# Optimization experiments

Measured on AMD Instinct MI355X. Metric: run time of the kernel, lower is better.

## Reference

```python
import jax, jax.numpy as jnp
import numpy as np

DIM = 192
WIN = 7
HEADS = 6
SHIFT = 3
HID = 4 * DIM


def _ln(x, w, b, eps=1e-5):
    m = jnp.mean(x, axis=-1, keepdims=True)
    v = jnp.var(x, axis=-1, keepdims=True)
    return (x - m) * jax.lax.rsqrt(v + eps) * w + b


def setup_inputs() -> dict:
    key = jax.random.key(0)
    ks = jax.random.split(key, 8)
    B, C, H, W = 16, DIM, 56, 56
    s = lambda k, shape, fan: jax.random.normal(k, shape, jnp.float32) * (1.0 / np.sqrt(fan))
    return {
        "x": jax.random.normal(ks[0], (B, C, H, W), jnp.float32),
        "norm1_w": jnp.ones((C,), jnp.float32),
        "norm1_b": jnp.zeros((C,), jnp.float32),
        "qkv_w": s(ks[1], (3 * C, C), C),
        "qkv_b": jnp.zeros((3 * C,), jnp.float32),
        "proj_w": s(ks[2], (C, C), C),
        "proj_b": jnp.zeros((C,), jnp.float32),
        "norm2_w": jnp.ones((C,), jnp.float32),
        "norm2_b": jnp.zeros((C,), jnp.float32),
        "fc1_w": s(ks[3], (HID, C), C),
        "fc1_b": jnp.zeros((HID,), jnp.float32),
        "fc2_w": s(ks[4], (C, HID), HID),
        "fc2_b": jnp.zeros((C,), jnp.float32),
    }


def reference(x, norm1_w, norm1_b, qkv_w, qkv_b, proj_w, proj_b,
              norm2_w, norm2_b, fc1_w, fc1_b, fc2_w, fc2_b):
    B, C, H, W = x.shape
    shift = SHIFT if (H > WIN and W > WIN) else 0
    shortcut = x

    xl = jnp.transpose(x, (0, 2, 3, 1))            # B,H,W,C
    xl = _ln(xl, norm1_w, norm1_b)
    if shift > 0:
        xl = jnp.roll(xl, shift=(-shift, -shift), axis=(1, 2))
    nH, nW = H // WIN, W // WIN
    xw = xl.reshape(B, nH, WIN, nW, WIN, C)
    xw = jnp.transpose(xw, (0, 1, 3, 2, 4, 5)).reshape(-1, WIN * WIN, C)

    # window attention
    Bw, N, _ = xw.shape
    dh = C // HEADS
    qkv = jnp.einsum('bnc,oc->bno', xw, qkv_w) + qkv_b
    qkv = qkv.reshape(Bw, N, 3, HEADS, dh)
    q, k, v = qkv[:, :, 0], qkv[:, :, 1], qkv[:, :, 2]   # Bw,N,H,dh
    scale = dh ** -0.5
    attn = jnp.einsum('bnhd,bmhd->bhnm', q, k) * scale
    attn = jax.nn.softmax(attn, axis=-1)
    out = jnp.einsum('bhnm,bmhd->bnhd', attn, v).reshape(Bw, N, C)
    out = jnp.einsum('bnc,oc->bno', out, proj_w) + proj_b

    # window reverse -> B,H,W,C
    xl = out.reshape(B, nH, nW, WIN, WIN, C)
    xl = jnp.transpose(xl, (0, 1, 3, 2, 4, 5)).reshape(B, H, W, C)
    if shift > 0:
        xl = jnp.roll(xl, shift=(shift, shift), axis=(1, 2))

    # norm2 + MLP (note: original has NO attention residual)
    xl = _ln(xl, norm2_w, norm2_b)
    h = jnp.einsum('bhwc,oc->bhwo', xl, fc1_w) + fc1_b
    h = jax.nn.gelu(h, approximate=False)
    h = jnp.einsum('bhwo,co->bhwc', h, fc2_w) + fc2_b
    return jnp.transpose(h, (0, 3, 1, 2)) + shortcut
```

## Files before the change

### kernel.cpp

```cpp
#include <hip/hip_runtime.h>
#include <hip/hip_bf16.h>

typedef __bf16 bf16_t;
typedef __bf16 bf16x4 __attribute__((ext_vector_type(4)));
typedef __bf16 bf16x8 __attribute__((ext_vector_type(8)));
typedef float f32x4 __attribute__((ext_vector_type(4)));

#define MFMA16(a, b, c) __builtin_amdgcn_mfma_f32_16x16x32_bf16((a), (b), (c), 0, 0, 0)

__device__ __forceinline__ void gl16(const bf16_t* g, void* l) {
    __builtin_amdgcn_global_load_lds(
        (const __attribute__((address_space(1))) void*)g,
        (__attribute__((address_space(3))) void*)l, 16, 0, 0);
}


__global__ __launch_bounds__(256) void k_cvt(const float* __restrict__ qkvw,
                                             const float* __restrict__ projw,
                                             const float* __restrict__ fc1w,
                                             const float* __restrict__ fc2w,
                                             bf16_t* __restrict__ dst)
{
    int i = blockIdx.x * 256 + threadIdx.x;
    if (i >= 442368) return;
    float v;
    if (i < 110592)      v = qkvw[i];
    else if (i < 147456) v = projw[i - 110592];
    else if (i < 294912) v = fc1w[i - 147456];
    else                 v = fc2w[i - 294912];
    dst[i] = (bf16_t)v;
}

__global__ __launch_bounds__(1024) void k_ln1(const float* __restrict__ x,
                                              const float* __restrict__ gam,
                                              const float* __restrict__ bet,
                                              bf16_t* __restrict__ xw)
{
    __shared__ float tile[56][193];
    __shared__ bf16_t obuf[56 * 192];
    const int bh = blockIdx.x;
    const int b = bh / 56, h = bh % 56;
    const int tid = threadIdx.x;

    {
        const int g = tid >> 4, u = tid & 15;
        const float* xb = x + (long)b * 602112 + (long)h * 56;
        if (u < 14) {
            #pragma unroll
            for (int k = 0; k < 3; ++k) {
                const int c = g + 64 * k;
                float4 v = *(const float4*)(xb + (long)c * 3136 + u * 4);
                tile[u * 4 + 0][c] = v.x;
                tile[u * 4 + 1][c] = v.y;
                tile[u * 4 + 2][c] = v.z;
                tile[u * 4 + 3][c] = v.w;
            }
        }
    }
    __syncthreads();

    const int wave = tid >> 6, lane = tid & 63;
    const float g0 = gam[lane], g1 = gam[lane + 64], g2 = gam[lane + 128];
    const float b0 = bet[lane], b1 = bet[lane + 64], b2 = bet[lane + 128];
    for (int wp = wave; wp < 56; wp += 16) {
        float v0 = tile[wp][lane], v1 = tile[wp][lane + 64], v2 = tile[wp][lane + 128];
        float s = v0 + v1 + v2;
        float sq = v0 * v0 + v1 * v1 + v2 * v2;
        #pragma unroll
        for (int d = 1; d < 64; d <<= 1) { s += __shfl_xor(s, d); sq += __shfl_xor(sq, d); }
        float mean = s * (1.f / 192.f);
        float var  = sq * (1.f / 192.f) - mean * mean;
        float rs = rsqrtf(var + 1e-5f);
        const int wr = (wp + 53) % 56;
        bf16_t* o = obuf + wr * 192;
        o[lane]       = (bf16_t)((v0 - mean) * rs * g0 + b0);
        o[lane + 64]  = (bf16_t)((v1 - mean) * rs * g1 + b1);
        o[lane + 128] = (bf16_t)((v2 - mean) * rs * g2 + b2);
    }
    __syncthreads();

    const int hr = (h + 53) % 56;
    const int nh = hr / 7, ii = hr % 7;
    const long rband = ((long)b * 64 + (long)nh * 8) * 49 + (long)ii * 7;
    const int4* src = (const int4*)obuf;
    for (int q = tid; q < 1344; q += 1024) {
        const int g = q / 168, u = q % 168;
        const int jj = u / 24, ci = u % 24;
        const long r = rband + (long)g * 49 + jj;
        ((int4*)xw)[r * 24 + ci] = src[(g * 7 + jj) * 24 + ci];
    }
}

template<int EPI>
__global__ __launch_bounds__(256) void k_gemm(const bf16_t* __restrict__ A,
                                              const bf16_t* __restrict__ W,
                                              const float* __restrict__ bias,
                                              bf16_t* __restrict__ outp,
                                              int M, int N, int K)
{
    __shared__ bf16_t As[128][64];
    __shared__ bf16_t Bs[64][64];
    const int tid = threadIdx.x;
    const int wv = tid >> 6, ln = tid & 63;
    const int lrow = ln & 15, lkg = ln >> 4;
    const int r7 = lrow & 7;
    const int wm = (wv >> 1) * 64, wn = (wv & 1) * 32;
    const long m0 = (long)blockIdx.x * 128;
    const int n0 = blockIdx.y * 64;

    f32x4 acc[4][2];
    #pragma unroll
    for (int mi = 0; mi < 4; ++mi)
        #pragma unroll
        for (int ni = 0; ni < 2; ++ni)
            #pragma unroll
            for (int rg = 0; rg < 4; ++rg) acc[mi][ni][rg] = 0.f;

    for (int k0 = 0; k0 < K; k0 += 64) {
        #pragma unroll
        for (int i = 0; i < 4; ++i) {
            const int off = ((wv * 4 + i) << 10) + ln * 16;
            const int row = off >> 7, c16 = (off >> 4) & 7;
            gl16(A + (m0 + row) * K + k0 + ((c16 ^ (row & 7)) << 3),
                 (char*)As + ((wv * 4 + i) << 10));
        }
        #pragma unroll
        for (int i = 0; i < 2; ++i) {
            const int off = ((wv * 2 + i) << 10) + ln * 16;
            const int row = off >> 7, c16 = (off >> 4) & 7;
            gl16(W + (long)(n0 + row) * K + k0 + ((c16 ^ (row & 7)) << 3),
                 (char*)Bs + ((wv * 2 + i) << 10));
        }
        __syncthreads();
        #pragma unroll
        for (int kk = 0; kk < 2; ++kk) {
            bf16x8 af[4], bfr[2];
            #pragma unroll
            for (int mi = 0; mi < 4; ++mi) {
                const int row = wm + mi * 16 + lrow;
                af[mi] = *(const bf16x8*)((const char*)As + row * 128
                           + ((((kk << 2) | lkg) ^ r7) << 4));
            }
            #pragma unroll
            for (int ni = 0; ni < 2; ++ni) {
                const int row = wn + ni * 16 + lrow;
                bfr[ni] = *(const bf16x8*)((const char*)Bs + row * 128
                           + ((((kk << 2) | lkg) ^ r7) << 4));
            }
            #pragma unroll
            for (int mi = 0; mi < 4; ++mi)
                #pragma unroll
                for (int ni = 0; ni < 2; ++ni)
                    acc[mi][ni] = MFMA16(bfr[ni], af[mi], acc[mi][ni]);
        }
        __syncthreads();
    }

    #pragma unroll
    for (int mi = 0; mi < 4; ++mi) {
        const long m = m0 + wm + mi * 16 + lrow;
        #pragma unroll
        for (int ni = 0; ni < 2; ++ni) {
            const int nb = n0 + wn + ni * 16 + lkg * 4;
            const float4 bv = *(const float4*)(bias + nb);
            float v[4] = { acc[mi][ni][0] + bv.x, acc[mi][ni][1] + bv.y,
                           acc[mi][ni][2] + bv.z, acc[mi][ni][3] + bv.w };
            bf16x4 o;
            #pragma unroll
            for (int rg = 0; rg < 4; ++rg) {
                float t = v[rg];
                if (EPI == 2) {
                    float t2 = fminf(t * (1.5957691216057308f
                                          + 0.07135481627f * t * t), 60.f);
                    float e = __expf(t2);
                    t = t * e / (e + 1.f);
                }
                o[rg] = (bf16_t)t;
            }
            *(bf16x4*)(outp + m * N + nb) = o;
        }
    }
}

__global__ __launch_bounds__(256) void k_proj_ln(const bf16_t* __restrict__ A,
                                                 const bf16_t* __restrict__ W,
                                                 const float* __restrict__ bias,
                                                 const float* __restrict__ gam,
                                                 const float* __restrict__ bet,
                                                 bf16_t* __restrict__ out)
{
    __shared__ bf16_t As[128][72];
    __shared__ bf16_t Bs[192][72];
    const int tid = threadIdx.x;
    const int wave = tid >> 6, lane = tid & 63;
    const int lrow = lane & 15, lkg = lane >> 4;
    const int wm = wave * 32;
    const long m0 = (long)blockIdx.x * 128;

    f32x4 acc[2][12];
    #pragma unroll
    for (int mi = 0; mi < 2; ++mi)
        #pragma unroll
        for (int ni = 0; ni < 12; ++ni)
            #pragma unroll
            for (int rg = 0; rg < 4; ++rg) acc[mi][ni][rg] = 0.f;

    for (int k0 = 0; k0 < 192; k0 += 64) {
        #pragma unroll
        for (int it = 0; it < 4; ++it) {
            int e = (tid + it * 256) * 8;
            int r = e >> 6, c = e & 63;
            *(int4*)(&As[r][c]) = *(const int4*)(A + (m0 + r) * 192 + (k0 + c));
        }
        #pragma unroll
        for (int it = 0; it < 6; ++it) {
            int e = (tid + it * 256) * 8;
            int r = e >> 6, c = e & 63;
            *(int4*)(&Bs[r][c]) = *(const int4*)(W + (long)r * 192 + (k0 + c));
        }
        __syncthreads();
        #pragma unroll
        for (int kk = 0; kk < 64; kk += 32) {
            bf16x8 af[2];
            #pragma unroll
            for (int mi = 0; mi < 2; ++mi)
                af[mi] = *(const bf16x8*)(&As[wm + mi * 16 + lrow][kk + lkg * 8]);
            #pragma unroll
            for (int ni = 0; ni < 12; ++ni) {
                bf16x8 bfr = *(const bf16x8*)(&Bs[ni * 16 + lrow][kk + lkg * 8]);
                acc[0][ni] = MFMA16(af[0], bfr, acc[0][ni]);
                acc[1][ni] = MFMA16(af[1], bfr, acc[1][ni]);
            }
        }
        __syncthreads();
    }

    float bv[12];
    #pragma unroll
    for (int ni = 0; ni < 12; ++ni) bv[ni] = bias[ni * 16 + lrow];

    #pragma unroll
    for (int mi = 0; mi < 2; ++mi) {
        #pragma unroll
        for (int rg = 0; rg < 4; ++rg) {
            float val[12];
            float s = 0.f, sq = 0.f;
            #pragma unroll
            for (int ni = 0; ni < 12; ++ni) {
                val[ni] = acc[mi][ni][rg] + bv[ni];
                s += val[ni];
                sq += val[ni] * val[ni];
            }
            #pragma unroll
            for (int d = 1; d < 16; d <<= 1) {
                s += __shfl_xor(s, d);
                sq += __shfl_xor(sq, d);
            }
            float mean = s * (1.f / 192.f);
            float var  = sq * (1.f / 192.f) - mean * mean;
            float rs = rsqrtf(var + 1e-5f);
            const long row = m0 + wm + mi * 16 + lkg * 4 + rg;
            bf16_t* orow = out + row * 192;
            #pragma unroll
            for (int ni = 0; ni < 12; ++ni) {
                const int col = ni * 16 + lrow;
                orow[col] = (bf16_t)((val[ni] - mean) * rs * gam[col] + bet[col]);
            }
        }
    }
}

__global__ __launch_bounds__(64) void k_attn(const bf16_t* __restrict__ qkv,
                                             bf16_t* __restrict__ aout)
{
    __shared__ bf16_t Pl[64][72];
    __shared__ bf16_t Vt[32][72];
    const int win = blockIdx.x, head = blockIdx.y;
    const int lane = threadIdx.x;
    const int lrow = lane & 15, lkg = lane >> 4;
    const bf16_t* base = qkv + (long)win * 28224 + head * 32;

    {
        const int m = lane;
        const int mc = (m < 49) ? m : 48;
        const int4* vr = (const int4*)(base + (long)mc * 576 + 384);
        #pragma unroll
        for (int c4 = 0; c4 < 4; ++c4) {
            int4 vv = vr[c4];
            if (m >= 49) vv = make_int4(0, 0, 0, 0);
            const bf16_t* pe = (const bf16_t*)&vv;
            #pragma unroll
            for (int e = 0; e < 8; ++e) Vt[c4 * 8 + e][m] = pe[e];
        }
    }

    bf16x8 z8;
    #pragma unroll
    for (int e = 0; e < 8; ++e) z8[e] = (bf16_t)0.f;
    bf16x8 qf[4], kf[4];
    #pragma unroll
    for (int t = 0; t < 4; ++t) {
        const int n = t * 16 + lrow;
        const int nc = (n < 49) ? n : 48;
        bf16x8 qv = *(const bf16x8*)(base + (long)nc * 576 + lkg * 8);
        bf16x8 kv = *(const bf16x8*)(base + (long)nc * 576 + 192 + lkg * 8);
        qf[t] = (n < 49) ? qv : z8;
        kf[t] = (n < 49) ? kv : z8;
    }
    f32x4 zf; zf[0] = zf[1] = zf[2] = zf[3] = 0.f;
    f32x4 S[4][4];
    #pragma unroll
    for (int mi = 0; mi < 4; ++mi)
        #pragma unroll
        for (int mj = 0; mj < 4; ++mj)
            S[mi][mj] = MFMA16(qf[mi], kf[mj], zf);

    const float scl = 0.17677669529663687f;
    #pragma unroll
    for (int mi = 0; mi < 4; ++mi) {
        #pragma unroll
        for (int rg = 0; rg < 4; ++rg) {
            float v0 = S[mi][0][rg] * scl;
            float v1 = S[mi][1][rg] * scl;
            float v2 = S[mi][2][rg] * scl;
            float v3 = (lrow == 0) ? S[mi][3][rg] * scl : -1e30f;
            float mx = fmaxf(fmaxf(v0, v1), fmaxf(v2, v3));
            #pragma unroll
            for (int d = 1; d < 16; d <<= 1) mx = fmaxf(mx, __shfl_xor(mx, d));
            float e0 = expf(v0 - mx), e1 = expf(v1 - mx), e2 = expf(v2 - mx);
            float e3 = (lrow == 0) ? expf(v3 - mx) : 0.f;
            float sm = e0 + e1 + e2 + e3;
            #pragma unroll
            for (int d = 1; d < 16; d <<= 1) sm += __shfl_xor(sm, d);
            float is = 1.f / sm;
            const int row = mi * 16 + lkg * 4 + rg;
            Pl[row][lrow]      = (bf16_t)(e0 * is);
            Pl[row][16 + lrow] = (bf16_t)(e1 * is);
            Pl[row][32 + lrow] = (bf16_t)(e2 * is);
            Pl[row][48 + lrow] = (bf16_t)(e3 * is);
        }
    }
    __syncthreads();

    f32x4 o[4][2];
    #pragma unroll
    for (int ni = 0; ni < 4; ++ni)
        #pragma unroll
        for (int di = 0; di < 2; ++di)
            #pragma unroll
            for (int rg = 0; rg < 4; ++rg) o[ni][di][rg] = 0.f;
    #pragma unroll
    for (int m0 = 0; m0 < 64; m0 += 32) {
        bf16x8 pf[4], vf[2];
        #pragma unroll
        for (int ni = 0; ni < 4; ++ni)
            pf[ni] = *(const bf16x8*)(&Pl[ni * 16 + lrow][m0 + lkg * 8]);
        #pragma unroll
        for (int di = 0; di < 2; ++di)
            vf[di] = *(const bf16x8*)(&Vt[di * 16 + lrow][m0 + lkg * 8]);
        #pragma unroll
        for (int ni = 0; ni < 4; ++ni)
            #pragma unroll
            for (int di = 0; di < 2; ++di)
                o[ni][di] = MFMA16(pf[ni], vf[di], o[ni][di]);
    }
    #pragma unroll
    for (int ni = 0; ni < 4; ++ni) {
        #pragma unroll
        for (int rg = 0; rg < 4; ++rg) {
            const int n = ni * 16 + lkg * 4 + rg;
            if (n < 49) {
                bf16_t* orow = aout + ((long)win * 49 + n) * 192 + head * 32;
                orow[lrow]      = (bf16_t)o[ni][0][rg];
                orow[16 + lrow] = (bf16_t)o[ni][1][rg];
            }
        }
    }
}

__global__ __launch_bounds__(1024) void k_final(const bf16_t* __restrict__ fb,
                                                const float* __restrict__ x,
                                                float* __restrict__ out)
{
    __shared__ float tile[56][199];
    const int bh = blockIdx.x;
    const int b = bh / 56, hq = bh % 56;
    const int tid = threadIdx.x;
    const int hr = (hq + 53) % 56;
    const int nh = hr / 7, ii = hr % 7;
    const long rband = ((long)b * 64 + (long)nh * 8) * 49 + (long)ii * 7;

    for (int q = tid; q < 1344; q += 1024) {
        const int g = q / 168, rem = q % 168;
        const int jj = rem / 24, ci = rem % 24;
        const long rr = rband + (long)g * 49 + jj;
        bf16x8 v = *(const bf16x8*)(fb + rr * 192 + ci * 8);
        const int wq = (g * 7 + jj + 3) % 56;
        #pragma unroll
        for (int e = 0; e < 8; ++e) tile[wq][ci * 8 + e] = (float)v[e];
    }
    __syncthreads();

    const int g = tid >> 4, u = tid & 15;
    if (u < 14) {
        #pragma unroll
        for (int k = 0; k < 3; ++k) {
            const int c = g + 64 * k;
            const long base = ((long)b * 192 + c) * 3136 + (long)hq * 56 + u * 4;
            float4 xv = *(const float4*)(x + base);
            float4 ov;
            ov.x = tile[u * 4 + 0][c] + xv.x;
            ov.y = tile[u * 4 + 1][c] + xv.y;
            ov.z = tile[u * 4 + 2][c] + xv.z;
            ov.w = tile[u * 4 + 3][c] + xv.w;
            *(float4*)(out + base) = ov;
        }
    }
}

extern "C" void kernel_launch(void* const* d_in, const int* in_sizes, int n_in,
                              void* d_out, int out_size, void* d_ws, size_t ws_size,
                              hipStream_t stream)
{
    const float* x     = (const float*)d_in[0];
    const float* n1w   = (const float*)d_in[1];
    const float* n1b   = (const float*)d_in[2];
    const float* qkvw  = (const float*)d_in[3];
    const float* qkvb  = (const float*)d_in[4];
    const float* projw = (const float*)d_in[5];
    const float* projb = (const float*)d_in[6];
    const float* n2w   = (const float*)d_in[7];
    const float* n2b   = (const float*)d_in[8];
    const float* fc1w  = (const float*)d_in[9];
    const float* fc1b  = (const float*)d_in[10];
    const float* fc2w  = (const float*)d_in[11];
    const float* fc2b  = (const float*)d_in[12];

    char* ws = (char*)d_ws;
    bf16_t* wqkv  = (bf16_t*)(ws);
    bf16_t* wproj = (bf16_t*)(ws + 221184);
    bf16_t* wfc1  = (bf16_t*)(ws + 294912);
    bf16_t* wfc2  = (bf16_t*)(ws + 589824);
    bf16_t* Xb    = (bf16_t*)(ws + 884736);
    bf16_t* QKV   = (bf16_t*)(ws + 20152320);
    bf16_t* Hb    = (bf16_t*)(ws + 77955072);
    bf16_t* H2    = (bf16_t*)(ws + 155025408);
    bf16_t* X2    = (bf16_t*)(ws + 174292992);

    k_cvt<<<1728, 256, 0, stream>>>(qkvw, projw, fc1w, fc2w, wqkv);
    k_ln1<<<896, 1024, 0, stream>>>(x, n1w, n1b, Xb);
    k_gemm<0><<<dim3(392, 9), 256, 0, stream>>>(Xb, wqkv, qkvb, QKV, 50176, 576, 192);
    k_attn<<<dim3(1024, 6), 64, 0, stream>>>(QKV, Xb);
    k_proj_ln<<<392, 256, 0, stream>>>(Xb, wproj, projb, n2w, n2b, X2);
    k_gemm<2><<<dim3(392, 12), 256, 0, stream>>>(X2, wfc1, fc1b, Hb, 50176, 768, 192);
    k_gemm<0><<<dim3(392, 3), 256, 0, stream>>>(Hb, wfc2, fc2b, H2, 50176, 192, 768);
    k_final<<<896, 1024, 0, stream>>>(H2, x, (float*)d_out);
}
```

Before: 219.7 us.

## Double-buffer GEMM LDS tiles and process several M tiles per block

Makes the GEMM kernel double-buffered: the next K tile (or the next M tile's first K tile) is loaded into a second LDS buffer while the current one is computed, leaving one barrier per step. For the K=192 GEMMs each block now handles four consecutive 128-row M tiles and writes the epilogue between them, so the grid shrinks fourfold. N and K become template constants. This hides global-load latency behind MFMA work and lowers per-block launch overhead, but doubles LDS use (possibly lowering occupancy) and gives fewer blocks for the QKV and fc1 launches.

```diff
diff --git a/kernel.cpp b/kernel.cpp
--- a/kernel.cpp
+++ b/kernel.cpp
@@ -91,23 +91,39 @@
     }
 }
 
-template<int EPI>
+template<int EPI, int N, int K, int G>
 __global__ __launch_bounds__(256) void k_gemm(const bf16_t* __restrict__ A,
                                               const bf16_t* __restrict__ W,
                                               const float* __restrict__ bias,
-                                              bf16_t* __restrict__ outp,
-                                              int M, int N, int K)
-{
-    __shared__ bf16_t As[128][64];
-    __shared__ bf16_t Bs[64][64];
+                                              bf16_t* __restrict__ outp)
+{
+    constexpr int NT = K / 64;
+    constexpr int NS = G * NT;
+    __shared__ bf16_t As[2][128 * 64];
+    __shared__ bf16_t Bs[2][64 * 64];
     const int tid = threadIdx.x;
     const int wv = tid >> 6, ln = tid & 63;
     const int lrow = ln & 15, lkg = ln >> 4;
     const int r7 = lrow & 7;
     const int wm = (wv >> 1) * 64, wn = (wv & 1) * 32;
-    const long m0 = (long)blockIdx.x * 128;
+    const long bm0 = (long)blockIdx.x * (G * 128);
     const int n0 = blockIdx.y * 64;
 
+    int arow[4], acol[4];
+    #pragma unroll
+    for (int i = 0; i < 4; ++i) {
+        const int off = ((wv * 4 + i) << 10) + ln * 16;
+        arow[i] = off >> 7;
+        acol[i] = (((off >> 4) & 7) ^ (arow[i] & 7)) << 3;
+    }
+    int brow[2], bcol[2];
+    #pragma unroll
+    for (int i = 0; i < 2; ++i) {
+        const int off = ((wv * 2 + i) << 10) + ln * 16;
+        brow[i] = off >> 7;
+        bcol[i] = (((off >> 4) & 7) ^ (brow[i] & 7)) << 3;
+    }
+
     f32x4 acc[4][2];
     #pragma unroll
     for (int mi = 0; mi < 4; ++mi)
@@ -116,35 +132,32 @@
             #pragma unroll
             for (int rg = 0; rg < 4; ++rg) acc[mi][ni][rg] = 0.f;
 
-    for (int k0 = 0; k0 < K; k0 += 64) {
-        #pragma unroll
-        for (int i = 0; i < 4; ++i) {
-            const int off = ((wv * 4 + i) << 10) + ln * 16;
-            const int row = off >> 7, c16 = (off >> 4) & 7;
-            gl16(A + (m0 + row) * K + k0 + ((c16 ^ (row & 7)) << 3),
-                 (char*)As + ((wv * 4 + i) << 10));
-        }
-        #pragma unroll
-        for (int i = 0; i < 2; ++i) {
-            const int off = ((wv * 2 + i) << 10) + ln * 16;
-            const int row = off >> 7, c16 = (off >> 4) & 7;
-            gl16(W + (long)(n0 + row) * K + k0 + ((c16 ^ (row & 7)) << 3),
-                 (char*)Bs + ((wv * 2 + i) << 10));
-        }
-        __syncthreads();
+    auto stage = [&](int buf, int g, int t) {
+        const long ab = (bm0 + (long)(g << 7)) * K + t * 64;
+        #pragma unroll
+        for (int i = 0; i < 4; ++i)
+            gl16(A + ab + arow[i] * K + acol[i],
+                 (char*)As[buf] + ((wv * 4 + i) << 10));
+        #pragma unroll
+        for (int i = 0; i < 2; ++i)
+            gl16(W + (long)(n0 + brow[i]) * K + t * 64 + bcol[i],
+                 (char*)Bs[buf] + ((wv * 2 + i) << 10));
+    };
+
+    auto compute = [&](int buf) {
         #pragma unroll
         for (int kk = 0; kk < 2; ++kk) {
             bf16x8 af[4], bfr[2];
             #pragma unroll
             for (int mi = 0; mi < 4; ++mi) {
                 const int row = wm + mi * 16 + lrow;
-                af[mi] = *(const bf16x8*)((const char*)As + row * 128
+                af[mi] = *(const bf16x8*)((const char*)As[buf] + row * 128
                            + ((((kk << 2) | lkg) ^ r7) << 4));
             }
             #pragma unroll
             for (int ni = 0; ni < 2; ++ni) {
                 const int row = wn + ni * 16 + lrow;
-                bfr[ni] = *(const bf16x8*)((const char*)Bs + row * 128
+                bfr[ni] = *(const bf16x8*)((const char*)Bs[buf] + row * 128
                            + ((((kk << 2) | lkg) ^ r7) << 4));
             }
             #pragma unroll
@@ -153,31 +166,52 @@
                 for (int ni = 0; ni < 2; ++ni)
                     acc[mi][ni] = MFMA16(bfr[ni], af[mi], acc[mi][ni]);
         }
-        __syncthreads();
-    }
-
-    #pragma unroll
-    for (int mi = 0; mi < 4; ++mi) {
-        const long m = m0 + wm + mi * 16 + lrow;
-        #pragma unroll
-        for (int ni = 0; ni < 2; ++ni) {
-            const int nb = n0 + wn + ni * 16 + lkg * 4;
-            const float4 bv = *(const float4*)(bias + nb);
-            float v[4] = { acc[mi][ni][0] + bv.x, acc[mi][ni][1] + bv.y,
-                           acc[mi][ni][2] + bv.z, acc[mi][ni][3] + bv.w };
-            bf16x4 o;
-            #pragma unroll
-            for (int rg = 0; rg < 4; ++rg) {
-                float t = v[rg];
-                if (EPI == 2) {
-                    float t2 = fminf(t * (1.5957691216057308f
-                                          + 0.07135481627f * t * t), 60.f);
-                    float e = __expf(t2);
-                    t = t * e / (e + 1.f);
+    };
+
+    stage(0, 0, 0);
+    __syncthreads();
+    int cur = 0;
+    #pragma unroll
+    for (int g = 0; g < G; ++g) {
+        #pragma unroll
+        for (int t = 0; t < NT; ++t) {
+            const int s = g * NT + t;
+            if (s + 1 < NS) {
+                const int t1 = (t + 1 == NT) ? 0 : t + 1;
+                const int g1 = (t + 1 == NT) ? g + 1 : g;
+                stage(cur ^ 1, g1, t1);
+            }
+            compute(cur);
+            if (t == NT - 1) {
+                #pragma unroll
+                for (int mi = 0; mi < 4; ++mi) {
+                    const long m = bm0 + (g << 7) + wm + mi * 16 + lrow;
+                    #pragma unroll
+                    for (int ni = 0; ni < 2; ++ni) {
+                        const int nb = n0 + wn + ni * 16 + lkg * 4;
+                        const float4 bv = *(const float4*)(bias + nb);
+                        float v[4] = { acc[mi][ni][0] + bv.x, acc[mi][ni][1] + bv.y,
+                                       acc[mi][ni][2] + bv.z, acc[mi][ni][3] + bv.w };
+                        bf16x4 o;
+                        #pragma unroll
+                        for (int rg = 0; rg < 4; ++rg) {
+                            float u = v[rg];
+                            if (EPI == 2) {
+                                float t2 = fminf(u * (1.5957691216057308f
+                                                      + 0.07135481627f * u * u), 60.f);
+                                float e = __expf(t2);
+                                u = u * e / (e + 1.f);
+                            }
+                            o[rg] = (bf16_t)u;
+                        }
+                        *(bf16x4*)(outp + m * N + nb) = o;
+                        #pragma unroll
+                        for (int rg = 0; rg < 4; ++rg) acc[mi][ni][rg] = 0.f;
+                    }
                 }
-                o[rg] = (bf16_t)t;
-            }
-            *(bf16x4*)(outp + m * N + nb) = o;
+            }
+            __syncthreads();
+            cur ^= 1;
         }
     }
 }
@@ -449,10 +483,10 @@
 
     k_cvt<<<1728, 256, 0, stream>>>(qkvw, projw, fc1w, fc2w, wqkv);
     k_ln1<<<896, 1024, 0, stream>>>(x, n1w, n1b, Xb);
-    k_gemm<0><<<dim3(392, 9), 256, 0, stream>>>(Xb, wqkv, qkvb, QKV, 50176, 576, 192);
+    k_gemm<0, 576, 192, 4><<<dim3(98, 9), 256, 0, stream>>>(Xb, wqkv, qkvb, QKV);
     k_attn<<<dim3(1024, 6), 64, 0, stream>>>(QKV, Xb);
     k_proj_ln<<<392, 256, 0, stream>>>(Xb, wproj, projb, n2w, n2b, X2);
-    k_gemm<2><<<dim3(392, 12), 256, 0, stream>>>(X2, wfc1, fc1b, Hb, 50176, 768, 192);
-    k_gemm<0><<<dim3(392, 3), 256, 0, stream>>>(Hb, wfc2, fc2b, H2, 50176, 192, 768);
+    k_gemm<2, 768, 192, 4><<<dim3(98, 12), 256, 0, stream>>>(X2, wfc1, fc1b, Hb);
+    k_gemm<0, 192, 768, 1><<<dim3(392, 3), 256, 0, stream>>>(Hb, wfc2, fc2b, H2);
     k_final<<<896, 1024, 0, stream>>>(H2, x, (float*)d_out);
 }
```

New measurement: 241.7 us. 1.1x slower.
